# Kernel tuning notes

Measured on AMD Instinct MI355X. Metric: run time of the kernel, lower is better.

The kernel has to match this reference:

```python
import jax, jax.numpy as jnp
import numpy as np

D_MODEL = 1024
N_HEAD = 16
B, C, S = 4, 4, 1024


def setup_inputs() -> dict:
    key = jax.random.key(0)
    ks = jax.random.split(key, 5)
    d = D_MODEL
    x = jax.random.normal(ks[0], (B, C, S, d), dtype=jnp.float32)
    scale = 1.0 / np.sqrt(d).astype(np.float32)

    def lin(k):
        return jax.random.normal(k, (d, d), dtype=jnp.float32) * scale

    return {
        "x": x,
        "wq": lin(ks[1]), "bq": jnp.zeros((d,), jnp.float32),
        "wk": lin(ks[2]), "bk": jnp.zeros((d,), jnp.float32),
        "wv": lin(ks[3]), "bv": jnp.zeros((d,), jnp.float32),
        "wo": lin(ks[4]), "bo": jnp.zeros((d,), jnp.float32),
    }


def reference(x, wq, bq, wk, bk, wv, bv, wo, bo):
    b, c, s, d = x.shape
    dh = d // N_HEAD
    nh = N_HEAD * c  # channels folded into heads, as in torch .view

    def proj(w, bias):
        # nn.Linear: y = x @ w.T + b  (w stored as [out, in])
        y = jnp.einsum('bcsd,ed->bcse', x, w) + bias
        # view(B, -1, n_head*C, d_head).transpose(1, 2) -> (B, nh, S, dh)
        return jnp.swapaxes(y.reshape(b, -1, nh, dh), 1, 2)

    # NOTE: original multiplies query by sqrt(d_head) (kept faithfully)
    q = proj(wq, bq) * jnp.sqrt(jnp.asarray(dh, x.dtype))
    k = proj(wk, bk)
    v = proj(wv, bv)

    attn = jax.nn.softmax(jnp.einsum('bhqd,bhkd->bhqk', q, k), axis=-1)
    o = jnp.einsum('bhqk,bhkd->bhqd', attn, v)          # (B, nh, S, dh)
    o = jnp.swapaxes(o, 1, 2).reshape(b, -1, N_HEAD * dh)  # (B, S*C, d)
    o = jnp.einsum('bnd,ed->bne', o, wo) + bo
    return o.reshape(b, c, -1, d)  # (B, C, S, d)
```

## Files before the change

kernel.cpp:

```cpp
#include <hip/hip_runtime.h>
#include <stdint.h>

typedef unsigned short u16;
typedef _Float16 f16;
typedef __attribute__((ext_vector_type(8))) _Float16 f16x8;
typedef __attribute__((ext_vector_type(4))) float f32x4;

__device__ __forceinline__ float exp2fast(float x) {
  return __builtin_amdgcn_exp2f(x);
}

__device__ __forceinline__ f32x4 mfma16(f16x8 a, f16x8 b, f32x4 c) {
  return __builtin_amdgcn_mfma_f32_16x16x32_f16(a, b, c, 0, 0, 0);
}

__device__ __forceinline__ u16 f2h(float f) {
  return __builtin_bit_cast(u16, (f16)f);
}

__device__ __forceinline__ void gld16(const void* g, void* l) {
  __builtin_amdgcn_global_load_lds(
      (const __attribute__((address_space(1))) unsigned int*)g,
      (__attribute__((address_space(3))) unsigned int*)l,
      16, 0, 0);
}

__global__ __launch_bounds__(256) void cvt_f32_f16(const float* __restrict__ in,
                                                   u16* __restrict__ out, int n4) {
  int stride = gridDim.x * blockDim.x;
  for (int i = blockIdx.x * blockDim.x + threadIdx.x; i < n4; i += stride) {
    float4 v = reinterpret_cast<const float4*>(in)[i];
    ushort4 o;
    o.x = f2h(v.x); o.y = f2h(v.y); o.z = f2h(v.z); o.w = f2h(v.w);
    reinterpret_cast<ushort4*>(out)[i] = o;
  }
}

__device__ __forceinline__ void stage_tile(const u16* __restrict__ M, int r0, int k0,
                                           u16* S, int wid, int lane) {
#pragma unroll
  for (int it = 0; it < 2; ++it) {
    int row = wid * 32 + it * 16 + (lane >> 2);
    int col = k0 + (lane & 3) * 8;
    gld16(M + (size_t)(r0 + row) * 1024 + col, S + wid * 1024 + it * 512);
  }
}

__global__ __launch_bounds__(256) void proj_qkv(
    const u16* __restrict__ xb,
    const u16* __restrict__ wqh, const u16* __restrict__ wkh, const u16* __restrict__ wvh,
    const float* __restrict__ bq, const float* __restrict__ bk, const float* __restrict__ bv,
    u16* __restrict__ Qf, u16* __restrict__ Kf, u16* __restrict__ Vt) {
  const int mat = blockIdx.z;
  const u16* __restrict__ w = (mat == 0) ? wqh : (mat == 1) ? wkh : wvh;
  const float* __restrict__ bias = (mat == 0) ? bq : (mat == 1) ? bk : bv;
  const int m0 = blockIdx.x * 128;
  const int n0 = blockIdx.y * 128;

  __shared__ __align__(16) u16 As[128 * 32];
  __shared__ __align__(16) u16 Bs[128 * 32];

  const int tid = threadIdx.x;
  const int lane = tid & 63;
  const int wid = tid >> 6;
  const int wr = wid >> 1, wc = wid & 1;
  const int qd = lane >> 4, lm = lane & 15;

  f32x4 acc[4][4];
#pragma unroll
  for (int i = 0; i < 4; ++i)
#pragma unroll
    for (int j = 0; j < 4; ++j) acc[i][j] = (f32x4){0.f, 0.f, 0.f, 0.f};

  stage_tile(xb, m0, 0, As, wid, lane);
  stage_tile(w, n0, 0, Bs, wid, lane);

  for (int kt = 0; kt < 32; ++kt) {
    __syncthreads();
    f16x8 af[4], bf[4];
#pragma unroll
    for (int i = 0; i < 4; ++i)
      af[i] = *reinterpret_cast<const f16x8*>(As + (wr * 64 + i * 16 + lm) * 32 + qd * 8);
#pragma unroll
    for (int j = 0; j < 4; ++j)
      bf[j] = *reinterpret_cast<const f16x8*>(Bs + (wc * 64 + j * 16 + lm) * 32 + qd * 8);
#pragma unroll
    for (int i = 0; i < 4; ++i)
#pragma unroll
      for (int j = 0; j < 4; ++j)
        acc[i][j] = mfma16(af[i], bf[j], acc[i][j]);
    __syncthreads();
    if (kt + 1 < 32) {
      stage_tile(xb, m0, (kt + 1) * 32, As, wid, lane);
      stage_tile(w, n0, (kt + 1) * 32, Bs, wid, lane);
    }
  }

  const float scale = (mat == 0) ? 11.5415603f : 1.0f;
#pragma unroll
  for (int i = 0; i < 4; ++i) {
#pragma unroll
    for (int r = 0; r < 4; ++r) {
      int R = m0 + wr * 64 + i * 16 + qd * 4 + r;
      int bb = R >> 12, n = R & 4095;
      int c = n >> 10, s = n & 1023;
      int rb = s & 3, t = s >> 2;
      int m = c * 256 + t;
#pragma unroll
      for (int j = 0; j < 4; ++j) {
        int e = n0 + wc * 64 + j * 16 + lm;
        int head = e >> 6, jj = e & 63;
        int h = rb * 16 + head;
        float val = (acc[i][j][r] + bias[e]) * scale;
        u16 hv = f2h(val);
        if (mat == 2) {
          Vt[(((size_t)bb * 64 + h) * 64 + jj) * 1024 + m] = hv;
        } else {
          size_t idx = (((size_t)bb * 64 + h) * 1024 + m) * 64 + jj;
          if (mat == 0) Qf[idx] = hv;
          else          Kf[idx] = hv;
        }
      }
    }
  }
}

__device__ __forceinline__ f16x8 lds_frag(const u16* base, int row, int blk) {
  return *reinterpret_cast<const f16x8*>(base + row * 64 + ((blk ^ (row & 7)) << 3));
}

__device__ __forceinline__ void stage_kv(const u16* __restrict__ Kh,
                                         const u16* __restrict__ Vh, int kc,
                                         u16* KsB, u16* VsB, int wv, int lane) {
  const int l8 = lane >> 3, sl = lane & 7;
  const int rb = wv * 16;
#pragma unroll
  for (int it = 0; it < 2; ++it) {
    int row = rb + it * 8 + l8;
    int gsl = sl ^ l8;
    gld16(Kh + (size_t)(kc * 64 + row) * 64 + gsl * 8, KsB + (rb + it * 8) * 64);
    gld16(Vh + (size_t)row * 1024 + kc * 64 + gsl * 8, VsB + (rb + it * 8) * 64);
  }
}

__global__ __launch_bounds__(256) void attn_kernel(
    const u16* __restrict__ Qf, const u16* __restrict__ Kf,
    const u16* __restrict__ Vt, u16* __restrict__ Of) {
  const int wgid = (blockIdx.x & 7) * 256 + (blockIdx.x >> 3);
  const int bh = wgid >> 3;
  const int m0 = (wgid & 7) * 128;
  const int b = bh >> 6, h = bh & 63;
  const int tid = threadIdx.x, lane = tid & 63, wv = tid >> 6;
  const int qd = lane >> 4, lm = lane & 15;

  __shared__ __align__(16) u16 Ks[2][64 * 64];
  __shared__ __align__(16) u16 Vs[2][64 * 64];

  const size_t hb = (size_t)(b * 64 + h);
  const u16* __restrict__ Qh = Qf + hb * 65536;
  const u16* __restrict__ Kh = Kf + hb * 65536;
  const u16* __restrict__ Vh = Vt + hb * 65536;

  f16x8 qf[2][2];
#pragma unroll
  for (int im = 0; im < 2; ++im)
#pragma unroll
    for (int ks = 0; ks < 2; ++ks)
      qf[im][ks] = *reinterpret_cast<const f16x8*>(
          Qh + (size_t)(m0 + wv * 32 + im * 16 + lm) * 64 + ks * 32 + qd * 8);

  f32x4 oa[2][4];
  float mrow[2] = {-1e30f, -1e30f};
  float lrow[2] = {0.f, 0.f};
#pragma unroll
  for (int im = 0; im < 2; ++im)
#pragma unroll
    for (int jf = 0; jf < 4; ++jf) oa[im][jf] = (f32x4){0.f, 0.f, 0.f, 0.f};

  stage_kv(Kh, Vh, 0, &Ks[0][0], &Vs[0][0], wv, lane);

  for (int kc = 0; kc < 16; ++kc) {
    const int buf = kc & 1;
    __syncthreads();
    if (kc + 1 < 16) stage_kv(Kh, Vh, kc + 1, &Ks[buf ^ 1][0], &Vs[buf ^ 1][0], wv, lane);

    f32x4 sc[2][4];
#pragma unroll
    for (int im = 0; im < 2; ++im)
#pragma unroll
      for (int nf = 0; nf < 4; ++nf) sc[im][nf] = (f32x4){0.f, 0.f, 0.f, 0.f};
#pragma unroll
    for (int ks = 0; ks < 2; ++ks) {
      f16x8 kfr[4];
#pragma unroll
      for (int nf = 0; nf < 4; ++nf)
        kfr[nf] = lds_frag(&Ks[buf][0], nf * 16 + lm, ks * 4 + qd);
#pragma unroll
      for (int im = 0; im < 2; ++im)
#pragma unroll
        for (int nf = 0; nf < 4; ++nf)
          sc[im][nf] = mfma16(kfr[nf], qf[im][ks], sc[im][nf]);
    }

    unsigned int pk[2][8];
#pragma unroll
    for (int im = 0; im < 2; ++im) {
      float pm = sc[im][0][0];
#pragma unroll
      for (int nf = 0; nf < 4; ++nf)
#pragma unroll
        for (int r = 0; r < 4; ++r) pm = fmaxf(pm, sc[im][nf][r]);
      pm = fmaxf(pm, __shfl_xor(pm, 16));
      pm = fmaxf(pm, __shfl_xor(pm, 32));
      if (__all(pm <= mrow[im] + 8.0f)) {
        float mn = mrow[im];
        float s = 0.f;
#pragma unroll
        for (int nf = 0; nf < 4; ++nf) {
          float p0 = exp2fast(sc[im][nf][0] - mn);
          float p1 = exp2fast(sc[im][nf][1] - mn);
          float p2 = exp2fast(sc[im][nf][2] - mn);
          float p3 = exp2fast(sc[im][nf][3] - mn);
          s += (p0 + p1) + (p2 + p3);
          pk[im][2 * nf + 0] = __builtin_bit_cast(unsigned int, __builtin_amdgcn_cvt_pkrtz(p0, p1));
          pk[im][2 * nf + 1] = __builtin_bit_cast(unsigned int, __builtin_amdgcn_cvt_pkrtz(p2, p3));
        }
        s += __shfl_xor(s, 16);
        s += __shfl_xor(s, 32);
        lrow[im] += s;
      } else {
        float mn = fmaxf(mrow[im], pm);
        float corr = exp2fast(mrow[im] - mn);
        mrow[im] = mn;
        float s = 0.f;
#pragma unroll
        for (int nf = 0; nf < 4; ++nf) {
          float p0 = exp2fast(sc[im][nf][0] - mn);
          float p1 = exp2fast(sc[im][nf][1] - mn);
          float p2 = exp2fast(sc[im][nf][2] - mn);
          float p3 = exp2fast(sc[im][nf][3] - mn);
          s += (p0 + p1) + (p2 + p3);
          pk[im][2 * nf + 0] = __builtin_bit_cast(unsigned int, __builtin_amdgcn_cvt_pkrtz(p0, p1));
          pk[im][2 * nf + 1] = __builtin_bit_cast(unsigned int, __builtin_amdgcn_cvt_pkrtz(p2, p3));
        }
        s += __shfl_xor(s, 16);
        s += __shfl_xor(s, 32);
        lrow[im] = lrow[im] * corr + s;
#pragma unroll
        for (int r = 0; r < 4; ++r) {
          float cb = __shfl(corr, qd * 4 + r);
#pragma unroll
          for (int jf = 0; jf < 4; ++jf) oa[im][jf][r] *= cb;
        }
      }
    }

#pragma unroll
    for (int ks = 0; ks < 2; ++ks) {
      f16x8 vfr[4];
#pragma unroll
      for (int jf = 0; jf < 4; ++jf)
        vfr[jf] = lds_frag(&Vs[buf][0], jf * 16 + lm, ks * 4 + qd);
#pragma unroll
      for (int im = 0; im < 2; ++im) {
        union { unsigned int w[4]; f16x8 hv; } pa;
#pragma unroll
        for (int w = 0; w < 4; ++w) {
          int srcl = (((2 * qd + (w >> 1)) & 3) << 4) + lm;
          unsigned int a0 = __shfl(pk[im][2 * (2 * ks + 0) + (w & 1)], srcl);
          unsigned int a1 = __shfl(pk[im][2 * (2 * ks + 1) + (w & 1)], srcl);
          pa.w[w] = (qd & 2) ? a1 : a0;
        }
#pragma unroll
        for (int jf = 0; jf < 4; ++jf)
          oa[im][jf] = mfma16(pa.hv, vfr[jf], oa[im][jf]);
      }
    }
  }

  const int rb = h >> 4, head = h & 15;
#pragma unroll
  for (int im = 0; im < 2; ++im) {
#pragma unroll
    for (int r = 0; r < 4; ++r) {
      float lb = __shfl(lrow[im], qd * 4 + r);
      float inv = 1.0f / lb;
      int mq = m0 + wv * 32 + im * 16 + qd * 4 + r;
      int c = mq >> 8, t = mq & 255;
      int s = t * 4 + rb;
      int n = c * 1024 + s;
#pragma unroll
      for (int jf = 0; jf < 4; ++jf) {
        int j = jf * 16 + lm;
        int f = head * 64 + j;
        Of[((size_t)b * 4096 + n) * 1024 + f] = f2h(oa[im][jf][r] * inv);
      }
    }
  }
}

__global__ __launch_bounds__(256) void out_gemm(
    const u16* __restrict__ Of, const u16* __restrict__ woh,
    const float* __restrict__ bo, float* __restrict__ out) {
  const int m0 = blockIdx.x * 128;
  const int n0 = blockIdx.y * 128;

  __shared__ __align__(16) u16 As[128 * 32];
  __shared__ __align__(16) u16 Bs[128 * 32];

  const int tid = threadIdx.x;
  const int lane = tid & 63;
  const int wid = tid >> 6;
  const int wr = wid >> 1, wc = wid & 1;
  const int qd = lane >> 4, lm = lane & 15;

  f32x4 acc[4][4];
#pragma unroll
  for (int i = 0; i < 4; ++i)
#pragma unroll
    for (int j = 0; j < 4; ++j) acc[i][j] = (f32x4){0.f, 0.f, 0.f, 0.f};

  stage_tile(Of, m0, 0, As, wid, lane);
  stage_tile(woh, n0, 0, Bs, wid, lane);

  for (int kt = 0; kt < 32; ++kt) {
    __syncthreads();
    f16x8 af[4], bf[4];
#pragma unroll
    for (int i = 0; i < 4; ++i)
      af[i] = *reinterpret_cast<const f16x8*>(As + (wr * 64 + i * 16 + lm) * 32 + qd * 8);
#pragma unroll
    for (int j = 0; j < 4; ++j)
      bf[j] = *reinterpret_cast<const f16x8*>(Bs + (wc * 64 + j * 16 + lm) * 32 + qd * 8);
#pragma unroll
    for (int i = 0; i < 4; ++i)
#pragma unroll
      for (int j = 0; j < 4; ++j)
        acc[i][j] = mfma16(af[i], bf[j], acc[i][j]);
    __syncthreads();
    if (kt + 1 < 32) {
      stage_tile(Of, m0, (kt + 1) * 32, As, wid, lane);
      stage_tile(woh, n0, (kt + 1) * 32, Bs, wid, lane);
    }
  }

#pragma unroll
  for (int i = 0; i < 4; ++i) {
#pragma unroll
    for (int r = 0; r < 4; ++r) {
      int R = m0 + wr * 64 + i * 16 + qd * 4 + r;
#pragma unroll
      for (int j = 0; j < 4; ++j) {
        int e = n0 + wc * 64 + j * 16 + lm;
        out[(size_t)R * 1024 + e] = acc[i][j][r] + bo[e];
      }
    }
  }
}

extern "C" void kernel_launch(void* const* d_in, const int* in_sizes, int n_in,
                              void* d_out, int out_size, void* d_ws, size_t ws_size,
                              hipStream_t stream) {
  const float* x  = (const float*)d_in[0];
  const float* wq = (const float*)d_in[1];
  const float* bq = (const float*)d_in[2];
  const float* wk = (const float*)d_in[3];
  const float* bk = (const float*)d_in[4];
  const float* wv = (const float*)d_in[5];
  const float* bv = (const float*)d_in[6];
  const float* wo = (const float*)d_in[7];
  const float* bo = (const float*)d_in[8];
  float* out = (float*)d_out;

  char* ws = (char*)d_ws;
  u16* xb  = (u16*)(ws + 0);
  u16* wqh = (u16*)(ws + 33554432);
  u16* wkh = (u16*)(ws + 35651584);
  u16* wvh = (u16*)(ws + 37748736);
  u16* woh = (u16*)(ws + 39845888);
  u16* Qfb = (u16*)(ws + 41943040);
  u16* Kfb = (u16*)(ws + 75497472);
  u16* Vtb = (u16*)(ws + 109051904);
  u16* Ofb = (u16*)(ws + 142606336);

  cvt_f32_f16<<<4096, 256, 0, stream>>>(x,  xb,  16777216 / 4);
  cvt_f32_f16<<<1024, 256, 0, stream>>>(wq, wqh, 1048576 / 4);
  cvt_f32_f16<<<1024, 256, 0, stream>>>(wk, wkh, 1048576 / 4);
  cvt_f32_f16<<<1024, 256, 0, stream>>>(wv, wvh, 1048576 / 4);
  cvt_f32_f16<<<1024, 256, 0, stream>>>(wo, woh, 1048576 / 4);

  proj_qkv<<<dim3(128, 8, 3), 256, 0, stream>>>(xb, wqh, wkh, wvh, bq, bk, bv,
                                                Qfb, Kfb, Vtb);
  attn_kernel<<<2048, 256, 0, stream>>>(Qfb, Kfb, Vtb, Ofb);
  out_gemm<<<dim3(128, 8), 256, 0, stream>>>(Ofb, woh, bo, out);
}
```

Before: 411.3 us.

## Double-buffer GEMM LDS tiles and XOR-swizzle layout in projection kernels

The QKV projection and output GEMMs now keep two shared-memory tile buffers. The next K-slice is loaded asynchronously while MFMAs run on the current one, and each k-step needs one barrier instead of two. The 16-byte granule position inside each row is XOR-swizzled on both the global-to-LDS load and the fragment read, to reduce LDS bank conflicts. Shared memory per block doubles, which may lower occupancy.

```diff
diff --git a/kernel.cpp b/kernel.cpp
--- a/kernel.cpp
+++ b/kernel.cpp
@@ -36,14 +36,66 @@
   }
 }
 
-__device__ __forceinline__ void stage_tile(const u16* __restrict__ M, int r0, int k0,
-                                           u16* S, int wid, int lane) {
-#pragma unroll
-  for (int it = 0; it < 2; ++it) {
-    int row = wid * 32 + it * 16 + (lane >> 2);
-    int col = k0 + (lane & 3) * 8;
-    gld16(M + (size_t)(r0 + row) * 1024 + col, S + wid * 1024 + it * 512);
-  }
+struct GemmCore {
+  u16* As;
+  u16* Bs;
+  const u16 *aS0, *aS1, *bS0, *bS1;
+  u16 *aD0, *aD1, *bD0, *bD1;
+  int aoff[4], boff[4];
+};
+
+__device__ __forceinline__ void core_init(GemmCore& c, u16* AsBase, u16* BsBase,
+                                          const u16* A, const u16* B,
+                                          int m0, int n0, int tid) {
+  const int lane = tid & 63;
+  const int wid = tid >> 6;
+  const int wr = wid >> 1, wc = wid & 1;
+  const int qd = lane >> 4, lm = lane & 15;
+
+  c.As = AsBase; c.Bs = BsBase;
+  const int srow = wid * 32 + (lane >> 2);
+  const int sgran = (lane & 3) ^ ((lane >> 3) & 3);
+  c.aS0 = A + (size_t)(m0 + srow) * 1024 + sgran * 8;
+  c.aS1 = c.aS0 + (size_t)16 * 1024;
+  c.bS0 = B + (size_t)(n0 + srow) * 1024 + sgran * 8;
+  c.bS1 = c.bS0 + (size_t)16 * 1024;
+  c.aD0 = AsBase + wid * 1024;       c.aD1 = c.aD0 + 512;
+  c.bD0 = BsBase + wid * 1024;       c.bD1 = c.bD0 + 512;
+
+  const int rg = (qd ^ ((lm >> 1) & 3)) * 8;
+#pragma unroll
+  for (int i = 0; i < 4; ++i) c.aoff[i] = (wr * 64 + i * 16 + lm) * 32 + rg;
+#pragma unroll
+  for (int j = 0; j < 4; ++j) c.boff[j] = (wc * 64 + j * 16 + lm) * 32 + rg;
+}
+
+__device__ __forceinline__ void core_stage(GemmCore& c, int buf) {
+  const int d = buf * 4096;
+  gld16(c.aS0, c.aD0 + d);
+  gld16(c.aS1, c.aD1 + d);
+  gld16(c.bS0, c.bD0 + d);
+  gld16(c.bS1, c.bD1 + d);
+}
+
+__device__ __forceinline__ void core_advance(GemmCore& c) {
+  c.aS0 += 32; c.aS1 += 32; c.bS0 += 32; c.bS1 += 32;
+}
+
+__device__ __forceinline__ void core_mfma(GemmCore& c, int buf, f32x4 (&acc)[4][4]) {
+  const u16* aB = c.As + buf * 4096;
+  const u16* bB = c.Bs + buf * 4096;
+  f16x8 af[4], bf[4];
+#pragma unroll
+  for (int i = 0; i < 4; ++i)
+    af[i] = *reinterpret_cast<const f16x8*>(aB + c.aoff[i]);
+#pragma unroll
+  for (int j = 0; j < 4; ++j)
+    bf[j] = *reinterpret_cast<const f16x8*>(bB + c.boff[j]);
+#pragma unroll
+  for (int i = 0; i < 4; ++i)
+#pragma unroll
+    for (int j = 0; j < 4; ++j)
+      acc[i][j] = mfma16(af[i], bf[j], acc[i][j]);
 }
 
 __global__ __launch_bounds__(256) void proj_qkv(
@@ -57,8 +109,8 @@
   const int m0 = blockIdx.x * 128;
   const int n0 = blockIdx.y * 128;
 
-  __shared__ __align__(16) u16 As[128 * 32];
-  __shared__ __align__(16) u16 Bs[128 * 32];
+  __shared__ __align__(16) u16 As[2][128 * 32];
+  __shared__ __align__(16) u16 Bs[2][128 * 32];
 
   const int tid = threadIdx.x;
   const int lane = tid & 63;
@@ -66,35 +118,27 @@
   const int wr = wid >> 1, wc = wid & 1;
   const int qd = lane >> 4, lm = lane & 15;
 
+  GemmCore c;
+  core_init(c, &As[0][0], &Bs[0][0], xb, w, m0, n0, tid);
+
   f32x4 acc[4][4];
 #pragma unroll
   for (int i = 0; i < 4; ++i)
 #pragma unroll
     for (int j = 0; j < 4; ++j) acc[i][j] = (f32x4){0.f, 0.f, 0.f, 0.f};
 
-  stage_tile(xb, m0, 0, As, wid, lane);
-  stage_tile(w, n0, 0, Bs, wid, lane);
-
-  for (int kt = 0; kt < 32; ++kt) {
+  core_stage(c, 0);
+  __syncthreads();
+
+  int buf = 0;
+  for (int kt = 0; kt < 31; ++kt) {
+    core_advance(c);
+    core_stage(c, buf ^ 1);
+    core_mfma(c, buf, acc);
     __syncthreads();
-    f16x8 af[4], bf[4];
-#pragma unroll
-    for (int i = 0; i < 4; ++i)
-      af[i] = *reinterpret_cast<const f16x8*>(As + (wr * 64 + i * 16 + lm) * 32 + qd * 8);
-#pragma unroll
-    for (int j = 0; j < 4; ++j)
-      bf[j] = *reinterpret_cast<const f16x8*>(Bs + (wc * 64 + j * 16 + lm) * 32 + qd * 8);
-#pragma unroll
-    for (int i = 0; i < 4; ++i)
-#pragma unroll
-      for (int j = 0; j < 4; ++j)
-        acc[i][j] = mfma16(af[i], bf[j], acc[i][j]);
-    __syncthreads();
-    if (kt + 1 < 32) {
-      stage_tile(xb, m0, (kt + 1) * 32, As, wid, lane);
-      stage_tile(w, n0, (kt + 1) * 32, Bs, wid, lane);
-    }
-  }
+    buf ^= 1;
+  }
+  core_mfma(c, buf, acc);
 
   const float scale = (mat == 0) ? 11.5415603f : 1.0f;
 #pragma unroll
@@ -103,9 +147,9 @@
     for (int r = 0; r < 4; ++r) {
       int R = m0 + wr * 64 + i * 16 + qd * 4 + r;
       int bb = R >> 12, n = R & 4095;
-      int c = n >> 10, s = n & 1023;
+      int cc = n >> 10, s = n & 1023;
       int rb = s & 3, t = s >> 2;
-      int m = c * 256 + t;
+      int m = cc * 256 + t;
 #pragma unroll
       for (int j = 0; j < 4; ++j) {
         int e = n0 + wc * 64 + j * 16 + lm;
@@ -305,8 +349,8 @@
   const int m0 = blockIdx.x * 128;
   const int n0 = blockIdx.y * 128;
 
-  __shared__ __align__(16) u16 As[128 * 32];
-  __shared__ __align__(16) u16 Bs[128 * 32];
+  __shared__ __align__(16) u16 As[2][128 * 32];
+  __shared__ __align__(16) u16 Bs[2][128 * 32];
 
   const int tid = threadIdx.x;
   const int lane = tid & 63;
@@ -314,35 +358,27 @@
   const int wr = wid >> 1, wc = wid & 1;
   const int qd = lane >> 4, lm = lane & 15;
 
+  GemmCore c;
+  core_init(c, &As[0][0], &Bs[0][0], Of, woh, m0, n0, tid);
+
   f32x4 acc[4][4];
 #pragma unroll
   for (int i = 0; i < 4; ++i)
 #pragma unroll
     for (int j = 0; j < 4; ++j) acc[i][j] = (f32x4){0.f, 0.f, 0.f, 0.f};
 
-  stage_tile(Of, m0, 0, As, wid, lane);
-  stage_tile(woh, n0, 0, Bs, wid, lane);
-
-  for (int kt = 0; kt < 32; ++kt) {
+  core_stage(c, 0);
+  __syncthreads();
+
+  int buf = 0;
+  for (int kt = 0; kt < 31; ++kt) {
+    core_advance(c);
+    core_stage(c, buf ^ 1);
+    core_mfma(c, buf, acc);
     __syncthreads();
-    f16x8 af[4], bf[4];
-#pragma unroll
-    for (int i = 0; i < 4; ++i)
-      af[i] = *reinterpret_cast<const f16x8*>(As + (wr * 64 + i * 16 + lm) * 32 + qd * 8);
-#pragma unroll
-    for (int j = 0; j < 4; ++j)
-      bf[j] = *reinterpret_cast<const f16x8*>(Bs + (wc * 64 + j * 16 + lm) * 32 + qd * 8);
-#pragma unroll
-    for (int i = 0; i < 4; ++i)
-#pragma unroll
-      for (int j = 0; j < 4; ++j)
-        acc[i][j] = mfma16(af[i], bf[j], acc[i][j]);
-    __syncthreads();
-    if (kt + 1 < 32) {
-      stage_tile(Of, m0, (kt + 1) * 32, As, wid, lane);
-      stage_tile(woh, n0, (kt + 1) * 32, Bs, wid, lane);
-    }
-  }
+    buf ^= 1;
+  }
+  core_mfma(c, buf, acc);
 
 #pragma unroll
   for (int i = 0; i < 4; ++i) {
```

After: 433.7 us. 5.5% more time.

## Use K=64 swizzled LDS tiles in GEMMs, batch weight casts, add MFMA priority

Applied to the files above, without the earlier changes.

The projection and output GEMMs now stage 64-wide K tiles into LDS with an XOR swizzle on the column groups. This halves the number of barrier pairs per tile and is meant to avoid LDS bank conflicts on fragment reads, at the cost of twice the LDS per block. The four weight-conversion launches are merged into one 2D-grid kernel to cut launch overhead. In the attention kernel, s_setprio is raised around the MFMA sections to favour matrix-issue scheduling.

```diff
diff --git a/kernel.cpp b/kernel.cpp
--- a/kernel.cpp
+++ b/kernel.cpp
@@ -36,13 +36,32 @@
   }
 }
 
-__device__ __forceinline__ void stage_tile(const u16* __restrict__ M, int r0, int k0,
-                                           u16* S, int wid, int lane) {
-#pragma unroll
-  for (int it = 0; it < 2; ++it) {
-    int row = wid * 32 + it * 16 + (lane >> 2);
-    int col = k0 + (lane & 3) * 8;
-    gld16(M + (size_t)(r0 + row) * 1024 + col, S + wid * 1024 + it * 512);
+struct Ptr8 {
+  const float *s0, *s1, *s2, *s3;
+  u16 *d0, *d1, *d2, *d3;
+};
+__global__ __launch_bounds__(256) void cvt4_f32_f16(Ptr8 p, int n4) {
+  const float* in = (blockIdx.y == 0) ? p.s0 : (blockIdx.y == 1) ? p.s1
+                    : (blockIdx.y == 2) ? p.s2 : p.s3;
+  u16* out = (blockIdx.y == 0) ? p.d0 : (blockIdx.y == 1) ? p.d1
+             : (blockIdx.y == 2) ? p.d2 : p.d3;
+  int stride = gridDim.x * blockDim.x;
+  for (int i = blockIdx.x * blockDim.x + threadIdx.x; i < n4; i += stride) {
+    float4 v = reinterpret_cast<const float4*>(in)[i];
+    ushort4 o;
+    o.x = f2h(v.x); o.y = f2h(v.y); o.z = f2h(v.z); o.w = f2h(v.w);
+    reinterpret_cast<ushort4*>(out)[i] = o;
+  }
+}
+
+__device__ __forceinline__ void stage64(const u16* __restrict__ M, int r0, int k0,
+                                        u16* S, int wid, int lane) {
+  const int l8 = lane >> 3;
+  const int col = k0 + (((lane & 7) ^ l8) << 3);
+#pragma unroll
+  for (int it = 0; it < 4; ++it) {
+    const int rowbase = wid * 32 + it * 8;
+    gld16(M + (size_t)(r0 + rowbase + l8) * 1024 + col, S + rowbase * 64);
   }
 }
 
@@ -57,8 +76,8 @@
   const int m0 = blockIdx.x * 128;
   const int n0 = blockIdx.y * 128;
 
-  __shared__ __align__(16) u16 As[128 * 32];
-  __shared__ __align__(16) u16 Bs[128 * 32];
+  __shared__ __align__(16) u16 As[128 * 64];
+  __shared__ __align__(16) u16 Bs[128 * 64];
 
   const int tid = threadIdx.x;
   const int lane = tid & 63;
@@ -72,27 +91,31 @@
 #pragma unroll
     for (int j = 0; j < 4; ++j) acc[i][j] = (f32x4){0.f, 0.f, 0.f, 0.f};
 
-  stage_tile(xb, m0, 0, As, wid, lane);
-  stage_tile(w, n0, 0, Bs, wid, lane);
-
-  for (int kt = 0; kt < 32; ++kt) {
+  stage64(xb, m0, 0, As, wid, lane);
+  stage64(w, n0, 0, Bs, wid, lane);
+
+  for (int kt = 0; kt < 16; ++kt) {
     __syncthreads();
-    f16x8 af[4], bf[4];
-#pragma unroll
-    for (int i = 0; i < 4; ++i)
-      af[i] = *reinterpret_cast<const f16x8*>(As + (wr * 64 + i * 16 + lm) * 32 + qd * 8);
-#pragma unroll
-    for (int j = 0; j < 4; ++j)
-      bf[j] = *reinterpret_cast<const f16x8*>(Bs + (wc * 64 + j * 16 + lm) * 32 + qd * 8);
-#pragma unroll
-    for (int i = 0; i < 4; ++i)
+#pragma unroll
+    for (int ks = 0; ks < 2; ++ks) {
+      const int gofs = ((ks * 4 + qd) ^ (lm & 7)) << 3;
+      f16x8 af[4], bf[4];
+#pragma unroll
+      for (int i = 0; i < 4; ++i)
+        af[i] = *reinterpret_cast<const f16x8*>(As + (wr * 64 + i * 16 + lm) * 64 + gofs);
 #pragma unroll
       for (int j = 0; j < 4; ++j)
-        acc[i][j] = mfma16(af[i], bf[j], acc[i][j]);
+        bf[j] = *reinterpret_cast<const f16x8*>(Bs + (wc * 64 + j * 16 + lm) * 64 + gofs);
+#pragma unroll
+      for (int i = 0; i < 4; ++i)
+#pragma unroll
+        for (int j = 0; j < 4; ++j)
+          acc[i][j] = mfma16(af[i], bf[j], acc[i][j]);
+    }
     __syncthreads();
-    if (kt + 1 < 32) {
-      stage_tile(xb, m0, (kt + 1) * 32, As, wid, lane);
-      stage_tile(w, n0, (kt + 1) * 32, Bs, wid, lane);
+    if (kt + 1 < 16) {
+      stage64(xb, m0, (kt + 1) * 64, As, wid, lane);
+      stage64(w, n0, (kt + 1) * 64, Bs, wid, lane);
     }
   }
 
@@ -103,9 +126,9 @@
     for (int r = 0; r < 4; ++r) {
       int R = m0 + wr * 64 + i * 16 + qd * 4 + r;
       int bb = R >> 12, n = R & 4095;
-      int c = n >> 10, s = n & 1023;
+      int cc = n >> 10, s = n & 1023;
       int rb = s & 3, t = s >> 2;
-      int m = c * 256 + t;
+      int m = cc * 256 + t;
 #pragma unroll
       for (int j = 0; j < 4; ++j) {
         int e = n0 + wc * 64 + j * 16 + lm;
@@ -189,6 +212,7 @@
     for (int im = 0; im < 2; ++im)
 #pragma unroll
       for (int nf = 0; nf < 4; ++nf) sc[im][nf] = (f32x4){0.f, 0.f, 0.f, 0.f};
+    __builtin_amdgcn_s_setprio(1);
 #pragma unroll
     for (int ks = 0; ks < 2; ++ks) {
       f16x8 kfr[4];
@@ -201,6 +225,7 @@
         for (int nf = 0; nf < 4; ++nf)
           sc[im][nf] = mfma16(kfr[nf], qf[im][ks], sc[im][nf]);
     }
+    __builtin_amdgcn_s_setprio(0);
 
     unsigned int pk[2][8];
 #pragma unroll
@@ -271,9 +296,11 @@
           unsigned int a1 = __shfl(pk[im][2 * (2 * ks + 1) + (w & 1)], srcl);
           pa.w[w] = (qd & 2) ? a1 : a0;
         }
+        __builtin_amdgcn_s_setprio(1);
 #pragma unroll
         for (int jf = 0; jf < 4; ++jf)
           oa[im][jf] = mfma16(pa.hv, vfr[jf], oa[im][jf]);
+        __builtin_amdgcn_s_setprio(0);
       }
     }
   }
@@ -305,8 +332,8 @@
   const int m0 = blockIdx.x * 128;
   const int n0 = blockIdx.y * 128;
 
-  __shared__ __align__(16) u16 As[128 * 32];
-  __shared__ __align__(16) u16 Bs[128 * 32];
+  __shared__ __align__(16) u16 As[128 * 64];
+  __shared__ __align__(16) u16 Bs[128 * 64];
 
   const int tid = threadIdx.x;
   const int lane = tid & 63;
@@ -320,27 +347,31 @@
 #pragma unroll
     for (int j = 0; j < 4; ++j) acc[i][j] = (f32x4){0.f, 0.f, 0.f, 0.f};
 
-  stage_tile(Of, m0, 0, As, wid, lane);
-  stage_tile(woh, n0, 0, Bs, wid, lane);
-
-  for (int kt = 0; kt < 32; ++kt) {
+  stage64(Of, m0, 0, As, wid, lane);
+  stage64(woh, n0, 0, Bs, wid, lane);
+
+  for (int kt = 0; kt < 16; ++kt) {
     __syncthreads();
-    f16x8 af[4], bf[4];
-#pragma unroll
-    for (int i = 0; i < 4; ++i)
-      af[i] = *reinterpret_cast<const f16x8*>(As + (wr * 64 + i * 16 + lm) * 32 + qd * 8);
-#pragma unroll
-    for (int j = 0; j < 4; ++j)
-      bf[j] = *reinterpret_cast<const f16x8*>(Bs + (wc * 64 + j * 16 + lm) * 32 + qd * 8);
-#pragma unroll
-    for (int i = 0; i < 4; ++i)
+#pragma unroll
+    for (int ks = 0; ks < 2; ++ks) {
+      const int gofs = ((ks * 4 + qd) ^ (lm & 7)) << 3;
+      f16x8 af[4], bf[4];
+#pragma unroll
+      for (int i = 0; i < 4; ++i)
+        af[i] = *reinterpret_cast<const f16x8*>(As + (wr * 64 + i * 16 + lm) * 64 + gofs);
 #pragma unroll
       for (int j = 0; j < 4; ++j)
-        acc[i][j] = mfma16(af[i], bf[j], acc[i][j]);
+        bf[j] = *reinterpret_cast<const f16x8*>(Bs + (wc * 64 + j * 16 + lm) * 64 + gofs);
+#pragma unroll
+      for (int i = 0; i < 4; ++i)
+#pragma unroll
+        for (int j = 0; j < 4; ++j)
+          acc[i][j] = mfma16(af[i], bf[j], acc[i][j]);
+    }
     __syncthreads();
-    if (kt + 1 < 32) {
-      stage_tile(Of, m0, (kt + 1) * 32, As, wid, lane);
-      stage_tile(woh, n0, (kt + 1) * 32, Bs, wid, lane);
+    if (kt + 1 < 16) {
+      stage64(Of, m0, (kt + 1) * 64, As, wid, lane);
+      stage64(woh, n0, (kt + 1) * 64, Bs, wid, lane);
     }
   }
 
@@ -383,11 +414,9 @@
   u16* Vtb = (u16*)(ws + 109051904);
   u16* Ofb = (u16*)(ws + 142606336);
 
-  cvt_f32_f16<<<4096, 256, 0, stream>>>(x,  xb,  16777216 / 4);
-  cvt_f32_f16<<<1024, 256, 0, stream>>>(wq, wqh, 1048576 / 4);
-  cvt_f32_f16<<<1024, 256, 0, stream>>>(wk, wkh, 1048576 / 4);
-  cvt_f32_f16<<<1024, 256, 0, stream>>>(wv, wvh, 1048576 / 4);
-  cvt_f32_f16<<<1024, 256, 0, stream>>>(wo, woh, 1048576 / 4);
+  cvt_f32_f16<<<4096, 256, 0, stream>>>(x, xb, 16777216 / 4);
+  Ptr8 p { wq, wk, wv, wo, wqh, wkh, wvh, woh };
+  cvt4_f32_f16<<<dim3(256, 4), 256, 0, stream>>>(p, 1048576 / 4);
 
   proj_qkv<<<dim3(128, 8, 3), 256, 0, stream>>>(xb, wqh, wkh, wvh, bq, bk, bv,
                                                 Qfb, Kfb, Vtb);
```

After: 384.4 us. -6.5%, faster.
